# Performance work log

Measured on AMD Instinct MI355X. Metric: run time of the kernel, lower is better.

Reference implementation:

```python
import jax, jax.numpy as jnp
import numpy as np

N = 50000      # nodes
E = 800000     # edges (avg degree 16)
IN = 128       # in_channels
H = 256        # hidden_channels
EPS = 1e-5     # BatchNorm eps


def setup_inputs() -> dict:
    key = jax.random.key(0)
    ks = iter(jax.random.split(key, 40))
    nrm = lambda shape, s: jax.random.normal(next(ks), shape, dtype=jnp.float32) * s
    d = {}
    d["x"] = nrm((N, IN), 1.0)
    d["edge_index"] = jax.random.randint(next(ks), (2, E), 0, N, dtype=jnp.int32)
    # SAGEConv layers: lin_l (neighbors, with bias) + lin_r (root, no bias); BatchNorm params
    dims = [(IN, H), (H, H), (H, H)]
    for i, (fi, fo) in enumerate(dims):
        s = 1.0 / np.sqrt(fi)
        d[f"w_l{i}"] = nrm((fo, fi), s)
        d[f"b_l{i}"] = nrm((fo,), s)
        d[f"w_r{i}"] = nrm((fo, fi), s)
        d[f"g{i}"] = jnp.ones((fo,), jnp.float32)
        d[f"be{i}"] = nrm((fo,), 0.1)
        d[f"rm{i}"] = nrm((fo,), 0.1)
        d[f"rv{i}"] = jax.random.uniform(next(ks), (fo,), jnp.float32, 0.5, 1.5)
    # predictor MLP: H->H, H->H//2, H//2->1
    for j, (fi, fo) in enumerate([(H, H), (H, H // 2), (H // 2, 1)], start=1):
        s = 1.0 / np.sqrt(fi)
        d[f"pw{j}"] = nrm((fo, fi), s)
        d[f"pb{j}"] = nrm((fo,), s)
    return d


def _sage(x, src, dst, w_l, b_l, w_r):
    # mean aggregation of neighbor messages (gather by src, scatter-add by dst)
    msum = jax.ops.segment_sum(x[src], dst, num_segments=N)       # [N, F]
    cnt = jax.ops.segment_sum(jnp.ones((src.shape[0], 1), x.dtype), dst, num_segments=N)
    mean = msum / jnp.maximum(cnt, 1.0)
    return mean @ w_l.T + b_l + x @ w_r.T


def _bn(x, g, be, rm, rv):
    return (x - rm) * jax.lax.rsqrt(rv + EPS) * g + be


def reference(x, edge_index,
              w_l0, b_l0, w_r0, g0, be0, rm0, rv0,
              w_l1, b_l1, w_r1, g1, be1, rm1, rv1,
              w_l2, b_l2, w_r2, g2, be2, rm2, rv2,
              pw1, pb1, pw2, pb2, pw3, pb3):
    src, dst = edge_index[0], edge_index[1]
    layers = [
        (w_l0, b_l0, w_r0, g0, be0, rm0, rv0),
        (w_l1, b_l1, w_r1, g1, be1, rm1, rv1),
        (w_l2, b_l2, w_r2, g2, be2, rm2, rv2),
    ]
    for (wl, bl, wr, g, be, rm, rv) in layers:
        x = _sage(x, src, dst, wl, bl, wr)
        x = jax.nn.relu(_bn(x, g, be, rm, rv))
        # dropout: identity in eval mode
    h = jax.nn.relu(x @ pw1.T + pb1)
    h = jax.nn.relu(h @ pw2.T + pb2)
    return jax.nn.sigmoid(h @ pw3.T + pb3)   # [N, 1]
```

## Files before the change

### kernel.cpp

```cpp
#include <hip/hip_runtime.h>
#include <hip/hip_fp16.h>

#define NNODES 50000
#define NEDGES 800000
#define CSTRIDE 64

typedef _Float16 f16;
typedef f16 f16x8 __attribute__((ext_vector_type(8)));
typedef f16 f16x4 __attribute__((ext_vector_type(4)));
typedef float f32x4 __attribute__((ext_vector_type(4)));

#define GLOAD_LDS16(g, l) __builtin_amdgcn_global_load_lds( \
    (const __attribute__((address_space(1))) void*)(g), \
    (__attribute__((address_space(3))) void*)(l), 16, 0, 0)


#define NPK 8
struct PackSeg { const float* w; f16* p; int FO; int K; };
struct AffSeg { const float *b, *g, *be, *rm, *rv; float *cs, *cb; int n; int isbn; };

struct FrontArgs {
    const int* src; const int* dst;
    int* cursor; int* csr;
    const float* x; f16* h0; int n4;
    const float* pw3; f16* pw3f;
    f16 *hA, *hB;
    PackSeg ps[NPK];
    AffSeg as[5];
};

__global__ void k_front(FrontArgs a) {
    int b = blockIdx.x, tid = threadIdx.x;
    if (b < 1024) {
        int t = b * 256 + tid;
        const int stride = 1024 * 256;
        int d[8], s[8], p[8];
        bool ok[8];
#pragma unroll
        for (int u = 0; u < 8; ++u) {
            int e = t + u * stride;
            ok[u] = (e < NEDGES);
            d[u] = ok[u] ? a.dst[e] : 0;
            s[u] = ok[u] ? a.src[e] : 0;
        }
#pragma unroll
        for (int u = 0; u < 8; ++u) p[u] = ok[u] ? atomicAdd(&a.cursor[d[u]], 1) : 0;
#pragma unroll
        for (int u = 0; u < 8; ++u)
            if (ok[u] && p[u] < CSTRIDE) a.csr[d[u] * CSTRIDE + p[u]] = s[u];
    } else if (b < 2624) {
        int i = (b - 1024) * 256 + tid, stride = 1600 * 256;
        for (; i < a.n4; i += stride) {
            float4 v = ((const float4*)a.x)[i];
            f16x4 o;
            o[0] = (f16)v.x; o[1] = (f16)v.y; o[2] = (f16)v.z; o[3] = (f16)v.w;
            ((f16x4*)a.h0)[i] = o;
        }
    } else if (b < 2880) {
        int gid = (b - 2624) * 256 + tid, gstride = 256 * 256;
        for (int sgi = 0; sgi < NPK; ++sgi) {
            PackSeg sg = a.ps[sgi];
            int total = sg.FO * sg.K / 8;
            int KS = sg.K >> 5;
            for (int t2 = gid; t2 < total; t2 += gstride) {
                int lane = t2 & 63;
                int tile = t2 >> 6;
                int ks = tile % KS, nt = tile / KS;
                int row = nt * 16 + (lane & 15);
                int col = ks * 32 + (lane >> 4) * 8;
                const float4* srcp = (const float4*)(sg.w + (size_t)row * sg.K + col);
                float4 v0 = srcp[0], v1 = srcp[1];
                f16x8 o;
                o[0] = (f16)v0.x; o[1] = (f16)v0.y; o[2] = (f16)v0.z; o[3] = (f16)v0.w;
                o[4] = (f16)v1.x; o[5] = (f16)v1.y; o[6] = (f16)v1.z; o[7] = (f16)v1.w;
                ((f16x8*)sg.p)[t2] = o;
            }
        }
    } else if (b < 2885) {
        AffSeg sg = a.as[b - 2880];
        if (tid < sg.n) {
            if (sg.isbn) {
                float sc = sg.g[tid] * rsqrtf(sg.rv[tid] + 1e-5f);
                sg.cs[tid] = sc;
                sg.cb[tid] = (sg.b[tid] - sg.rm[tid]) * sc + sg.be[tid];
            } else {
                sg.cs[tid] = 1.0f;
                sg.cb[tid] = sg.b[tid];
            }
        }
    } else {
        f16x4 z = {};
        if (tid < 32) {
            ((f16x4*)(a.h0 + (size_t)NNODES * 128))[tid] = z;
        } else if (tid < 96) {
            ((f16x4*)(a.hA + (size_t)NNODES * 256))[tid - 32] = z;
        } else if (tid < 160) {
            ((f16x4*)(a.hB + (size_t)NNODES * 256))[tid - 96] = z;
        } else if (tid < 192) {
            int i = tid - 160;
            float4 v = ((const float4*)a.pw3)[i];
            f16x4 o;
            o[0] = (f16)v.x; o[1] = (f16)v.y; o[2] = (f16)v.z; o[3] = (f16)v.w;
            ((f16x4*)a.pw3f)[i] = o;
        }
    }
}

template <int F>
__global__ __launch_bounds__(256) void k_aggregate(
    const f16* __restrict__ h, const int* __restrict__ deg,
    const int* __restrict__ csr, f16* __restrict__ mean) {
    constexpr int LPN = F / 8;
    constexpr int NPW = 64 / LPN;
    int tid = threadIdx.x;
    int wave = tid >> 6, lane = tid & 63;
    int node = blockIdx.x * (4 * NPW) + wave * NPW + lane / LPN;
    int t = lane % LPN;
    int d = deg[node];
    if (d > CSTRIDE) d = CSTRIDE;
    int beg = node * CSTRIDE;
    const f16x8* hb = (const f16x8*)h;
    float acc[8] = {0.f, 0.f, 0.f, 0.f, 0.f, 0.f, 0.f, 0.f};

    int r = 0;
    for (; r + 16 <= d; r += 16) {
        int iA[8], iB[8];
#pragma unroll
        for (int u = 0; u < 8; ++u) iA[u] = csr[beg + r + u];
#pragma unroll
        for (int u = 0; u < 8; ++u) iB[u] = csr[beg + r + 8 + u];
        f16x8 vA[8], vB[8];
#pragma unroll
        for (int u = 0; u < 8; ++u) vA[u] = hb[(size_t)iA[u] * LPN + t];
#pragma unroll
        for (int u = 0; u < 8; ++u) vB[u] = hb[(size_t)iB[u] * LPN + t];
#pragma unroll
        for (int u = 0; u < 8; ++u)
#pragma unroll
            for (int e = 0; e < 8; ++e) acc[e] += (float)vA[u][e];
#pragma unroll
        for (int u = 0; u < 8; ++u)
#pragma unroll
            for (int e = 0; e < 8; ++e) acc[e] += (float)vB[u][e];
    }
    if (r < d) {
        int iA[8], iB[8];
#pragma unroll
        for (int u = 0; u < 8; ++u) {
            int raw = csr[beg + r + u];
            iA[u] = (r + u < d) ? raw : NNODES;
        }
#pragma unroll
        for (int u = 0; u < 8; ++u) {
            int raw = (r + 8 + u < CSTRIDE) ? csr[beg + r + 8 + u] : 0;
            iB[u] = (r + 8 + u < d) ? raw : NNODES;
        }
        f16x8 vA[8], vB[8];
#pragma unroll
        for (int u = 0; u < 8; ++u) vA[u] = hb[(size_t)iA[u] * LPN + t];
#pragma unroll
        for (int u = 0; u < 8; ++u) vB[u] = hb[(size_t)iB[u] * LPN + t];
#pragma unroll
        for (int u = 0; u < 8; ++u)
#pragma unroll
            for (int e = 0; e < 8; ++e) acc[e] += (float)vA[u][e];
#pragma unroll
        for (int u = 0; u < 8; ++u)
#pragma unroll
            for (int e = 0; e < 8; ++e) acc[e] += (float)vB[u][e];
    }

    float inv = (d > 0) ? 1.0f / (float)d : 0.0f;
    f16x8 o;
#pragma unroll
    for (int e = 0; e < 8; ++e) o[e] = (f16)(acc[e] * inv);
    ((f16x8*)mean)[(size_t)node * LPN + t] = o;
}

template <int FO, bool FUSE>
__global__ __launch_bounds__(FO * 2, 4) void k_gemm(
    const f16* __restrict__ A1, const f16* __restrict__ A2,
    const f16* __restrict__ W1p, const f16* __restrict__ W2p,
    const float* __restrict__ cs, const float* __restrict__ cb,
    f16* __restrict__ out, const f16* __restrict__ w3,
    const float* __restrict__ pb3, float* __restrict__ outF,
    int M, int K) {
    constexpr int WC = FO / 64;
    constexpr int NT = FO * 2;
    __shared__ f16 As[2][128 * 64];
    __shared__ float smF[WC][128];
    int tid = threadIdx.x;
    int lane = tid & 63;
    int wave = tid >> 6;
    int wr = wave / WC, wc = wave % WC;
    int m0 = blockIdx.x * 128;
    int lrow = lane & 15;
    int kof8 = (lane >> 4) * 8;
    int KC1 = K >> 6;
    int KS = K >> 5;
    int NC = A2 ? KC1 * 2 : KC1;

    auto stage = [&](int buf, int c) {
        int ph = (c >= KC1) ? 1 : 0;
        const char* Ab = (const char*)(ph ? A2 : A1);
        int kb0 = ((c - ph * KC1) << 6) * 2;
        char* Al = (char*)&As[buf][0];
#pragma unroll
        for (int u0 = 0; u0 < 1024; u0 += NT) {
            int u = u0 + tid;
            int row = u >> 3;
            int kb = (u & 7) * 16;
            int grow = m0 + row; if (grow > M - 1) grow = M - 1;
            GLOAD_LDS16(Ab + (size_t)grow * (K * 2) + kb0 + (kb ^ ((row & 7) << 4)), Al + u * 16);
        }
    };

    f32x4 acc[4][4] = {};

    stage(0, 0);
    __syncthreads();

    for (int c = 0; c < NC; ++c) {
        int ph = (c >= KC1) ? 1 : 0;
        const f16x8* Wp = (const f16x8*)(ph ? W2p : W1p);
        int cl = c - ph * KC1;
        f16x8 b[2][4];
#pragma unroll
        for (int kk = 0; kk < 2; ++kk) {
            int ks = cl * 2 + kk;
#pragma unroll
            for (int ni = 0; ni < 4; ++ni) {
                int nt = wc * 4 + ni;
                b[kk][ni] = Wp[((size_t)nt * KS + ks) * 64 + lane];
            }
        }
        if (c + 1 < NC) stage((c + 1) & 1, c + 1);
        const char* Al = (const char*)&As[c & 1][0];
#pragma unroll
        for (int kk = 0; kk < 2; ++kk) {
            int kb = kof8 * 2 + kk * 64;
            f16x8 a[4];
#pragma unroll
            for (int mi = 0; mi < 4; ++mi) {
                int r = wr * 64 + mi * 16 + lrow;
                a[mi] = *(const f16x8*)(Al + r * 128 + (kb ^ ((r & 7) << 4)));
            }
#pragma unroll
            for (int mi = 0; mi < 4; ++mi)
#pragma unroll
                for (int ni = 0; ni < 4; ++ni)
                    acc[mi][ni] = __builtin_amdgcn_mfma_f32_16x16x32_f16(a[mi], b[kk][ni], acc[mi][ni], 0, 0, 0);
        }
        __syncthreads();
    }

    if constexpr (!FUSE) {
        int rquad = (lane >> 4) * 4;
#pragma unroll
        for (int mi = 0; mi < 4; ++mi) {
#pragma unroll
            for (int ni = 0; ni < 4; ++ni) {
                int col = wc * 64 + ni * 16 + (lane & 15);
                float s = cs[col], cc = cb[col];
#pragma unroll
                for (int r = 0; r < 4; ++r) {
                    int row = m0 + wr * 64 + mi * 16 + rquad + r;
                    if (row < M) {
                        float v = acc[mi][ni][r] * s + cc;
                        v = fmaxf(v, 0.f);
                        out[(size_t)row * FO + col] = (f16)v;
                    }
                }
            }
        }
    } else {
        float b3 = pb3[0];
        float rsum[4][4] = {};
#pragma unroll
        for (int ni = 0; ni < 4; ++ni) {
            int col = wc * 64 + ni * 16 + (lane & 15);
            float w3v = (float)w3[col];
            float cbv = cb[col];
#pragma unroll
            for (int mi = 0; mi < 4; ++mi)
#pragma unroll
                for (int r = 0; r < 4; ++r)
                    rsum[mi][r] += fmaxf(acc[mi][ni][r] + cbv, 0.f) * w3v;
        }
#pragma unroll
        for (int mi = 0; mi < 4; ++mi)
#pragma unroll
            for (int r = 0; r < 4; ++r) {
                float s = rsum[mi][r];
                s += __shfl_xor(s, 1); s += __shfl_xor(s, 2);
                s += __shfl_xor(s, 4); s += __shfl_xor(s, 8);
                if ((lane & 15) == 0)
                    smF[wc][wr * 64 + mi * 16 + (lane >> 4) * 4 + r] = s;
            }
        __syncthreads();
        if (tid < 128) {
            int row = m0 + tid;
            if (row < M) {
                float s = b3;
#pragma unroll
                for (int w = 0; w < WC; ++w) s += smF[w][tid];
                outF[row] = 1.0f / (1.0f + expf(-s));
            }
        }
    }
}


extern "C" void kernel_launch(void* const* d_in, const int* in_sizes, int n_in,
                              void* d_out, int out_size, void* d_ws, size_t ws_size,
                              hipStream_t stream) {
    const float* x = (const float*)d_in[0];
    const int* ei = (const int*)d_in[1];
    const int* src = ei;
    const int* dst = ei + NEDGES;
    const float* w_l[3] = {(const float*)d_in[2], (const float*)d_in[9], (const float*)d_in[16]};
    const float* b_l[3] = {(const float*)d_in[3], (const float*)d_in[10], (const float*)d_in[17]};
    const float* w_r[3] = {(const float*)d_in[4], (const float*)d_in[11], (const float*)d_in[18]};
    const float* g[3]  = {(const float*)d_in[5], (const float*)d_in[12], (const float*)d_in[19]};
    const float* be[3] = {(const float*)d_in[6], (const float*)d_in[13], (const float*)d_in[20]};
    const float* rm[3] = {(const float*)d_in[7], (const float*)d_in[14], (const float*)d_in[21]};
    const float* rv[3] = {(const float*)d_in[8], (const float*)d_in[15], (const float*)d_in[22]};
    const float* pw1 = (const float*)d_in[23]; const float* pb1 = (const float*)d_in[24];
    const float* pw2 = (const float*)d_in[25]; const float* pb2 = (const float*)d_in[26];
    const float* pw3 = (const float*)d_in[27]; const float* pb3 = (const float*)d_in[28];

    char* wsb = (char*)d_ws;
    size_t o = 0;
    auto alloc = [&](size_t b) { size_t r = o; o = (o + b + 255) & ~(size_t)255; return r; };

    size_t cur_off = alloc(NNODES * 4);
    int* cursor = (int*)(wsb + cur_off);
    int* csr    = (int*)(wsb + alloc((size_t)NNODES * CSTRIDE * 4));
    f16* h0   = (f16*)(wsb + alloc((size_t)(NNODES + 1) * 128 * 2));
    f16* hA   = (f16*)(wsb + alloc((size_t)(NNODES + 1) * 256 * 2));
    f16* hB   = (f16*)(wsb + alloc((size_t)(NNODES + 1) * 256 * 2));
    f16* mean = (f16*)(wsb + alloc((size_t)NNODES * 256 * 2));
    f16* wl0p = (f16*)(wsb + alloc(256 * 128 * 2));
    f16* wr0p = (f16*)(wsb + alloc(256 * 128 * 2));
    f16* wl1p = (f16*)(wsb + alloc(256 * 256 * 2));
    f16* wr1p = (f16*)(wsb + alloc(256 * 256 * 2));
    f16* wl2p = (f16*)(wsb + alloc(256 * 256 * 2));
    f16* wr2p = (f16*)(wsb + alloc(256 * 256 * 2));
    f16* pw1p = (f16*)(wsb + alloc(256 * 256 * 2));
    f16* pw2p = (f16*)(wsb + alloc(128 * 256 * 2));
    f16* pw3f = (f16*)(wsb + alloc(128 * 2));
    float* csv[5]; float* cbv[5];
    for (int i = 0; i < 5; ++i) {
        csv[i] = (float*)(wsb + alloc(256 * 4));
        cbv[i] = (float*)(wsb + alloc(256 * 4));
    }

    hipMemsetAsync(wsb + cur_off, 0, NNODES * 4, stream);
    FrontArgs fa;
    fa.src = src; fa.dst = dst;
    fa.cursor = cursor; fa.csr = csr;
    fa.x = x; fa.h0 = h0; fa.n4 = NNODES * 128 / 4;
    fa.pw3 = pw3; fa.pw3f = pw3f;
    fa.hA = hA; fa.hB = hB;
    fa.ps[0] = {w_l[0], wl0p, 256, 128};
    fa.ps[1] = {w_r[0], wr0p, 256, 128};
    fa.ps[2] = {w_l[1], wl1p, 256, 256};
    fa.ps[3] = {w_r[1], wr1p, 256, 256};
    fa.ps[4] = {w_l[2], wl2p, 256, 256};
    fa.ps[5] = {w_r[2], wr2p, 256, 256};
    fa.ps[6] = {pw1,    pw1p, 256, 256};
    fa.ps[7] = {pw2,    pw2p, 128, 256};
    for (int i = 0; i < 3; ++i)
        fa.as[i] = {b_l[i], g[i], be[i], rm[i], rv[i], csv[i], cbv[i], 256, 1};
    fa.as[3] = {pb1, nullptr, nullptr, nullptr, nullptr, csv[3], cbv[3], 256, 0};
    fa.as[4] = {pb2, nullptr, nullptr, nullptr, nullptr, csv[4], cbv[4], 128, 0};
    k_front<<<2886, 256, 0, stream>>>(fa);

    int gm = (NNODES + 127) / 128;

    k_aggregate<128><<<3125, 256, 0, stream>>>(h0, cursor, csr, mean);
    k_gemm<256, false><<<gm, 512, 0, stream>>>(mean, h0, wl0p, wr0p, csv[0], cbv[0], hA,
                                               nullptr, nullptr, nullptr, NNODES, 128);
    k_aggregate<256><<<6250, 256, 0, stream>>>(hA, cursor, csr, mean);
    k_gemm<256, false><<<gm, 512, 0, stream>>>(mean, hA, wl1p, wr1p, csv[1], cbv[1], hB,
                                               nullptr, nullptr, nullptr, NNODES, 256);
    k_aggregate<256><<<6250, 256, 0, stream>>>(hB, cursor, csr, mean);
    k_gemm<256, false><<<gm, 512, 0, stream>>>(mean, hB, wl2p, wr2p, csv[2], cbv[2], hA,
                                               nullptr, nullptr, nullptr, NNODES, 256);
    k_gemm<256, false><<<gm, 512, 0, stream>>>(hA, nullptr, pw1p, nullptr, csv[3], cbv[3], hB,
                                               nullptr, nullptr, nullptr, NNODES, 256);
    k_gemm<128, true><<<gm, 256, 0, stream>>>(hB, nullptr, pw2p, nullptr, csv[4], cbv[4], nullptr,
                                              pw3f, pb3, (float*)d_out, NNODES, 256);
}
```

Measured before the change: 305.7 us.

## Store CSR neighbor indices as u16 and restructure front kernel as grid-stride

Neighbor indices in the padded CSR are stored as 16-bit values, since node ids stay below 65536. This halves CSR write and read traffic and lets the aggregate kernel fetch eight indices with one 16-byte vector load instead of eight scalar loads. The front kernel no longer partitions blocks by role. All 2048 blocks now grid-stride over edge insertion, x conversion and weight packing in turn. This ties correctness to the node count staying under 65536 and changes load balance across the front-stage jobs.

```diff
diff --git a/kernel.cpp b/kernel.cpp
--- a/kernel.cpp
+++ b/kernel.cpp
@@ -4,10 +4,13 @@
 #define NNODES 50000
 #define NEDGES 800000
 #define CSTRIDE 64
+#define FG 2048
 
 typedef _Float16 f16;
+typedef unsigned short u16;
 typedef f16 f16x8 __attribute__((ext_vector_type(8)));
 typedef f16 f16x4 __attribute__((ext_vector_type(4)));
+typedef u16 u16x8 __attribute__((ext_vector_type(8)));
 typedef float f32x4 __attribute__((ext_vector_type(4)));
 
 #define GLOAD_LDS16(g, l) __builtin_amdgcn_global_load_lds( \
@@ -21,7 +24,7 @@
 
 struct FrontArgs {
     const int* src; const int* dst;
-    int* cursor; int* csr;
+    int* cursor; u16* csr;
     const float* x; f16* h0; int n4;
     const float* pw3; f16* pw3f;
     f16 *hA, *hB;
@@ -29,55 +32,50 @@
     AffSeg as[5];
 };
 
-__global__ void k_front(FrontArgs a) {
+__global__ __launch_bounds__(256) void k_front(FrontArgs a) {
     int b = blockIdx.x, tid = threadIdx.x;
-    if (b < 1024) {
-        int t = b * 256 + tid;
-        const int stride = 1024 * 256;
-        int d[8], s[8], p[8];
-        bool ok[8];
-#pragma unroll
-        for (int u = 0; u < 8; ++u) {
-            int e = t + u * stride;
-            ok[u] = (e < NEDGES);
-            d[u] = ok[u] ? a.dst[e] : 0;
-            s[u] = ok[u] ? a.src[e] : 0;
-        }
-#pragma unroll
-        for (int u = 0; u < 8; ++u) p[u] = ok[u] ? atomicAdd(&a.cursor[d[u]], 1) : 0;
-#pragma unroll
-        for (int u = 0; u < 8; ++u)
-            if (ok[u] && p[u] < CSTRIDE) a.csr[d[u] * CSTRIDE + p[u]] = s[u];
-    } else if (b < 2624) {
-        int i = (b - 1024) * 256 + tid, stride = 1600 * 256;
-        for (; i < a.n4; i += stride) {
-            float4 v = ((const float4*)a.x)[i];
-            f16x4 o;
-            o[0] = (f16)v.x; o[1] = (f16)v.y; o[2] = (f16)v.z; o[3] = (f16)v.w;
-            ((f16x4*)a.h0)[i] = o;
-        }
-    } else if (b < 2880) {
-        int gid = (b - 2624) * 256 + tid, gstride = 256 * 256;
-        for (int sgi = 0; sgi < NPK; ++sgi) {
-            PackSeg sg = a.ps[sgi];
-            int total = sg.FO * sg.K / 8;
-            int KS = sg.K >> 5;
-            for (int t2 = gid; t2 < total; t2 += gstride) {
-                int lane = t2 & 63;
-                int tile = t2 >> 6;
-                int ks = tile % KS, nt = tile / KS;
-                int row = nt * 16 + (lane & 15);
-                int col = ks * 32 + (lane >> 4) * 8;
-                const float4* srcp = (const float4*)(sg.w + (size_t)row * sg.K + col);
-                float4 v0 = srcp[0], v1 = srcp[1];
-                f16x8 o;
-                o[0] = (f16)v0.x; o[1] = (f16)v0.y; o[2] = (f16)v0.z; o[3] = (f16)v0.w;
-                o[4] = (f16)v1.x; o[5] = (f16)v1.y; o[6] = (f16)v1.z; o[7] = (f16)v1.w;
-                ((f16x8*)sg.p)[t2] = o;
-            }
-        }
-    } else if (b < 2885) {
-        AffSeg sg = a.as[b - 2880];
+    int gtid = b * 256 + tid;
+    const int NT = FG * 256;
+
+    {
+        int e0 = gtid, e1 = gtid + NT;
+        bool k0 = e0 < NEDGES, k1 = e1 < NEDGES;
+        int d0 = k0 ? a.dst[e0] : 0, s0 = k0 ? a.src[e0] : 0;
+        int d1 = k1 ? a.dst[e1] : 0, s1 = k1 ? a.src[e1] : 0;
+        int p0 = k0 ? atomicAdd(&a.cursor[d0], 1) : 0;
+        int p1 = k1 ? atomicAdd(&a.cursor[d1], 1) : 0;
+        if (k0 && p0 < CSTRIDE) a.csr[d0 * CSTRIDE + p0] = (u16)s0;
+        if (k1 && p1 < CSTRIDE) a.csr[d1 * CSTRIDE + p1] = (u16)s1;
+    }
+
+    for (int i = gtid; i < a.n4; i += NT) {
+        float4 v = ((const float4*)a.x)[i];
+        f16x4 o;
+        o[0] = (f16)v.x; o[1] = (f16)v.y; o[2] = (f16)v.z; o[3] = (f16)v.w;
+        ((f16x4*)a.h0)[i] = o;
+    }
+
+    for (int sgi = 0; sgi < NPK; ++sgi) {
+        PackSeg sg = a.ps[sgi];
+        int total = sg.FO * sg.K / 8;
+        int KS = sg.K >> 5;
+        for (int t2 = gtid; t2 < total; t2 += NT) {
+            int lane = t2 & 63;
+            int tile = t2 >> 6;
+            int ks = tile % KS, nt = tile / KS;
+            int row = nt * 16 + (lane & 15);
+            int col = ks * 32 + (lane >> 4) * 8;
+            const float4* srcp = (const float4*)(sg.w + (size_t)row * sg.K + col);
+            float4 v0 = srcp[0], v1 = srcp[1];
+            f16x8 o;
+            o[0] = (f16)v0.x; o[1] = (f16)v0.y; o[2] = (f16)v0.z; o[3] = (f16)v0.w;
+            o[4] = (f16)v1.x; o[5] = (f16)v1.y; o[6] = (f16)v1.z; o[7] = (f16)v1.w;
+            ((f16x8*)sg.p)[t2] = o;
+        }
+    }
+
+    if (b < 5) {
+        AffSeg sg = a.as[b];
         if (tid < sg.n) {
             if (sg.isbn) {
                 float sc = sg.g[tid] * rsqrtf(sg.rv[tid] + 1e-5f);
@@ -88,7 +86,7 @@
                 sg.cb[tid] = sg.b[tid];
             }
         }
-    } else {
+    } else if (b == 5) {
         f16x4 z = {};
         if (tid < 32) {
             ((f16x4*)(a.h0 + (size_t)NNODES * 128))[tid] = z;
@@ -109,7 +107,7 @@
 template <int F>
 __global__ __launch_bounds__(256) void k_aggregate(
     const f16* __restrict__ h, const int* __restrict__ deg,
-    const int* __restrict__ csr, f16* __restrict__ mean) {
+    const u16* __restrict__ csr, f16* __restrict__ mean) {
     constexpr int LPN = F / 8;
     constexpr int NPW = 64 / LPN;
     int tid = threadIdx.x;
@@ -124,37 +122,30 @@
 
     int r = 0;
     for (; r + 16 <= d; r += 16) {
+        u16x8 rA = *(const u16x8*)&csr[beg + r];
+        u16x8 rB = *(const u16x8*)&csr[beg + r + 8];
+        f16x8 vA[8], vB[8];
+#pragma unroll
+        for (int u = 0; u < 8; ++u) vA[u] = hb[(size_t)rA[u] * LPN + t];
+#pragma unroll
+        for (int u = 0; u < 8; ++u) vB[u] = hb[(size_t)rB[u] * LPN + t];
+#pragma unroll
+        for (int u = 0; u < 8; ++u)
+#pragma unroll
+            for (int e = 0; e < 8; ++e) acc[e] += (float)vA[u][e];
+#pragma unroll
+        for (int u = 0; u < 8; ++u)
+#pragma unroll
+            for (int e = 0; e < 8; ++e) acc[e] += (float)vB[u][e];
+    }
+    if (r < d) {
+        u16x8 rA = *(const u16x8*)&csr[beg + r];
+        u16x8 rB = *(const u16x8*)&csr[beg + r + 8];
         int iA[8], iB[8];
 #pragma unroll
-        for (int u = 0; u < 8; ++u) iA[u] = csr[beg + r + u];
-#pragma unroll
-        for (int u = 0; u < 8; ++u) iB[u] = csr[beg + r + 8 + u];
-        f16x8 vA[8], vB[8];
-#pragma unroll
-        for (int u = 0; u < 8; ++u) vA[u] = hb[(size_t)iA[u] * LPN + t];
-#pragma unroll
-        for (int u = 0; u < 8; ++u) vB[u] = hb[(size_t)iB[u] * LPN + t];
-#pragma unroll
-        for (int u = 0; u < 8; ++u)
-#pragma unroll
-            for (int e = 0; e < 8; ++e) acc[e] += (float)vA[u][e];
-#pragma unroll
-        for (int u = 0; u < 8; ++u)
-#pragma unroll
-            for (int e = 0; e < 8; ++e) acc[e] += (float)vB[u][e];
-    }
-    if (r < d) {
-        int iA[8], iB[8];
-#pragma unroll
-        for (int u = 0; u < 8; ++u) {
-            int raw = csr[beg + r + u];
-            iA[u] = (r + u < d) ? raw : NNODES;
-        }
-#pragma unroll
-        for (int u = 0; u < 8; ++u) {
-            int raw = (r + 8 + u < CSTRIDE) ? csr[beg + r + 8 + u] : 0;
-            iB[u] = (r + 8 + u < d) ? raw : NNODES;
-        }
+        for (int u = 0; u < 8; ++u) iA[u] = (r + u < d) ? (int)rA[u] : NNODES;
+#pragma unroll
+        for (int u = 0; u < 8; ++u) iB[u] = (r + 8 + u < d) ? (int)rB[u] : NNODES;
         f16x8 vA[8], vB[8];
 #pragma unroll
         for (int u = 0; u < 8; ++u) vA[u] = hb[(size_t)iA[u] * LPN + t];
@@ -335,7 +326,7 @@
 
     size_t cur_off = alloc(NNODES * 4);
     int* cursor = (int*)(wsb + cur_off);
-    int* csr    = (int*)(wsb + alloc((size_t)NNODES * CSTRIDE * 4));
+    u16* csr    = (u16*)(wsb + alloc((size_t)NNODES * CSTRIDE * 2));
     f16* h0   = (f16*)(wsb + alloc((size_t)(NNODES + 1) * 128 * 2));
     f16* hA   = (f16*)(wsb + alloc((size_t)(NNODES + 1) * 256 * 2));
     f16* hB   = (f16*)(wsb + alloc((size_t)(NNODES + 1) * 256 * 2));
@@ -374,7 +365,7 @@
         fa.as[i] = {b_l[i], g[i], be[i], rm[i], rv[i], csv[i], cbv[i], 256, 1};
     fa.as[3] = {pb1, nullptr, nullptr, nullptr, nullptr, csv[3], cbv[3], 256, 0};
     fa.as[4] = {pb2, nullptr, nullptr, nullptr, nullptr, csv[4], cbv[4], 128, 0};
-    k_front<<<2886, 256, 0, stream>>>(fa);
+    k_front<<<FG, 256, 0, stream>>>(fa);
 
     int gm = (NNODES + 127) / 128;
 
```

Result: faster. 285.8 us (-6.5%).
